# Performance work log

Hardware: AMD Instinct MI355X
Metric: run time of the kernel (lower is better)

The kernel has to match this reference:

```python
import jax, jax.numpy as jnp
import numpy as np
import math

B, T, C = 4, 2048, 1024
H = 16
D = C // H

def setup_inputs() -> dict:
    key = jax.random.key(0)
    k1, k2, k3 = jax.random.split(key, 3)
    x = jax.random.normal(k1, (B, T, C), dtype=jnp.float32)
    w_attn = jax.random.normal(k2, (3 * C, C), dtype=jnp.float32) * (1.0 / math.sqrt(C))
    b_attn = jnp.zeros((3 * C,), dtype=jnp.float32)
    w_proj = jax.random.normal(k3, (C, C), dtype=jnp.float32) * (1.0 / math.sqrt(C))
    b_proj = jnp.zeros((C,), dtype=jnp.float32)
    return {"x": x, "w_attn": w_attn, "b_attn": b_attn, "w_proj": w_proj, "b_proj": b_proj}

def reference(x, w_attn, b_attn, w_proj, b_proj):
    Bq, Tq, Cq = x.shape
    qkv = x @ w_attn.T + b_attn                      # [B,T,3C]
    q, k, v = jnp.split(qkv, 3, axis=-1)
    q = q.reshape(Bq, Tq, H, D).transpose(0, 2, 1, 3)  # [B,H,T,D]
    k = k.reshape(Bq, Tq, H, D).transpose(0, 2, 1, 3)
    v = v.reshape(Bq, Tq, H, D).transpose(0, 2, 1, 3)
    att = jnp.einsum('bhqd,bhkd->bhqk', q, k) * (1.0 / math.sqrt(D))
    causal = jnp.tril(jnp.ones((Tq, Tq), dtype=bool))
    att = jnp.where(causal[None, None], att, -jnp.inf)
    att = jax.nn.softmax(att, axis=-1)
    y = jnp.einsum('bhqk,bhkd->bhqd', att, v)          # [B,H,T,D]
    y = y.transpose(0, 2, 1, 3).reshape(Bq, Tq, Cq)
    return y @ w_proj.T + b_proj
```

## Files before the change

kernel.cpp:

```cpp
#include <hip/hip_runtime.h>
#include <hip/hip_bf16.h>


typedef __hip_bfloat16 bf16;
typedef __attribute__((ext_vector_type(8))) short bf16x8;
typedef __attribute__((ext_vector_type(4))) float f32x4;
typedef __attribute__((ext_vector_type(16))) float f32x16;

#define MFMA16(a, b, c) __builtin_amdgcn_mfma_f32_16x16x32_bf16(a, b, c, 0, 0, 0)
#define MFMA32(a, b, c) __builtin_amdgcn_mfma_f32_32x32x16_bf16(a, b, c, 0, 0, 0)
#define GLOAD_LDS(g, l) __builtin_amdgcn_global_load_lds( \
    (const __attribute__((address_space(1))) void*)(g),    \
    (__attribute__((address_space(3))) void*)(l), 16, 0, 0)

constexpr int Bn = 4, Tn = 2048, Cn = 1024, Hn = 16, Dn = 64;
constexpr size_t HT_ELEMS = (size_t)64 * Tn * Dn;
constexpr float QSCALE = 0.18033688011112042f;

__device__ __forceinline__ short f2bf(float f) {
    unsigned u = __float_as_uint(f);
    return (short)((u + 0x7FFF + ((u >> 16) & 1)) >> 16);
}
__device__ __forceinline__ bf16 bfbits(short s) { bf16 b; __builtin_memcpy(&b, &s, 2); return b; }

__device__ __forceinline__ unsigned cvtpk_bf16(float lo, float hi) {
    unsigned r;
    asm("v_cvt_pk_bf16_f32 %0, %1, %2" : "=v"(r) : "v"(lo), "v"(hi));
    return r;
}
__device__ __forceinline__ void permswap(unsigned& a, unsigned& b) {
#if __has_builtin(__builtin_amdgcn_permlane32_swap)
    auto r = __builtin_amdgcn_permlane32_swap(a, b, false, false);
    a = (unsigned)r[0]; b = (unsigned)r[1];
#else
    asm("v_permlane32_swap_b32 %0, %1" : "+v"(a), "+v"(b));
#endif
}
__device__ __forceinline__ bf16x8 pack4(unsigned w0, unsigned w1, unsigned w2, unsigned w3) {
    union { unsigned u[4]; bf16x8 v; } t;
    t.u[0] = w0; t.u[1] = w1; t.u[2] = w2; t.u[3] = w3;
    return t.v;
}

__global__ __launch_bounds__(256) void cast3_kernel(
    const float* __restrict__ x, const float* __restrict__ wa,
    const float* __restrict__ wp, bf16* __restrict__ out)
{
    size_t i = (size_t)blockIdx.x * 256 + threadIdx.x;
    const float* src; size_t off;
    if (i < 1048576)      { src = x;  off = i; }
    else if (i < 1441792) { src = wa; off = i - 1048576; }
    else                  { src = wp; off = i - 1441792; }
    const float4* p = (const float4*)(src + off * 8);
    float4 a = p[0], b = p[1];
    bf16x8 r;
    r[0] = f2bf(a.x); r[1] = f2bf(a.y); r[2] = f2bf(a.z); r[3] = f2bf(a.w);
    r[4] = f2bf(b.x); r[5] = f2bf(b.y); r[6] = f2bf(b.z); r[7] = f2bf(b.w);
    *(bf16x8*)(out + i * 8) = r;
}

__global__ __launch_bounds__(256) void qkv_gemm128(
    const bf16* __restrict__ Am, const bf16* __restrict__ Wm,
    const float* __restrict__ bias,
    bf16* __restrict__ qo, bf16* __restrict__ ko, bf16* __restrict__ vo)
{
    constexpr int K = 1024;
    __shared__ bf16 As[4096], Bs[4096];
    const int tid = threadIdx.x;
    const int lane = tid & 63, w = tid >> 6;
    const int row = lane & 15, quad = lane >> 4;
    const unsigned bid = blockIdx.x;
    const int x8 = bid & 7, l = bid >> 3;
    const int tm = (x8 >> 1) * 16 + l / 12;
    const int tn = (x8 & 1) * 12 + l % 12;
    const int m0 = tm * 128, n0 = tn * 128;

    const int srow = tid >> 2, skch = tid & 3;
    const bf16* ag0 = Am + (size_t)(m0 + srow) * K + skch * 8;
    const bf16* ag1 = ag0 + (size_t)64 * K;
    const bf16* wg0 = Wm + (size_t)(n0 + srow) * K + skch * 8;
    const bf16* wg1 = wg0 + (size_t)64 * K;
    bf16* asl0 = As + tid * 8;  bf16* asl1 = As + 2048 + tid * 8;
    bf16* bsl0 = Bs + tid * 8;  bf16* bsl1 = Bs + 2048 + tid * 8;

    f32x4 acc[4][4];
    #pragma unroll
    for (int i = 0; i < 4; i++)
        #pragma unroll
        for (int j = 0; j < 4; j++) acc[i][j] = {0, 0, 0, 0};

    const int r0 = (w >> 1) * 64, c0 = (w & 1) * 64;

    for (int k0 = 0; k0 < K; k0 += 32) {
        __syncthreads();
        GLOAD_LDS(ag0 + k0, asl0);
        GLOAD_LDS(ag1 + k0, asl1);
        GLOAD_LDS(wg0 + k0, bsl0);
        GLOAD_LDS(wg1 + k0, bsl1);
        __syncthreads();
        bf16x8 af[4], bfv[4];
        #pragma unroll
        for (int it = 0; it < 4; it++)
            af[it] = *(const bf16x8*)(As + (r0 + it * 16 + row) * 32 + quad * 8);
        #pragma unroll
        for (int jt = 0; jt < 4; jt++)
            bfv[jt] = *(const bf16x8*)(Bs + (c0 + jt * 16 + row) * 32 + quad * 8);
        #pragma unroll
        for (int it = 0; it < 4; it++)
            #pragma unroll
            for (int jt = 0; jt < 4; jt++)
                acc[it][jt] = MFMA16(af[it], bfv[jt], acc[it][jt]);
    }

    #pragma unroll
    for (int it = 0; it < 4; it++)
    #pragma unroll
    for (int jt = 0; jt < 4; jt++)
    #pragma unroll
    for (int r = 0; r < 4; r++) {
        int m = m0 + r0 + it * 16 + quad * 4 + r;
        int n = n0 + c0 + jt * 16 + row;
        float val = acc[it][jt][r] + bias[n];
        int which = n >> 10, cc = n & 1023;
        if (which == 0) val *= QSCALE;
        bf16 bv = bfbits(f2bf(val));
        int h = cc >> 6, d = cc & 63;
        int b = m >> 11, t = m & 2047;
        int bh = b * Hn + h;
        if (which == 0)      qo[((size_t)bh * Tn + t) * Dn + d] = bv;
        else if (which == 1) ko[((size_t)bh * Tn + t) * Dn + d] = bv;
        else                 vo[((size_t)bh * 64 + (t >> 5)) * 2048 + (size_t)d * 32 + (t & 31)] = bv;
    }
}

__global__ __launch_bounds__(256, 4) void attn_kernel(
    const bf16* __restrict__ qbp, const bf16* __restrict__ kbp,
    const bf16* __restrict__ vtb, bf16* __restrict__ ob)
{
    __shared__ __align__(128) bf16 SB[4][2048];
    __shared__ float lbufw[4][32];
    const int tid  = threadIdx.x;
    const int lane = tid & 63;
    const int w    = tid >> 6;
    const int l31  = lane & 31, hl = lane >> 5;
    const int bid  = blockIdx.x;
    const int qid  = bid & 7;
    const int idx  = bid >> 3;
    const int bh   = qid * 8 + (idx & 7);
    const int pair = idx >> 3;

    const int stage_off = w * 1024 + (lane >> 3) * 128
                        + (((lane & 7) ^ ((lane >> 3) & 7)) << 4);
    const int kxor = (l31 & 7) << 4;
    const int sxor = ((l31 >> 1) & 7) << 4;

    const bf16* Q  = qbp + (size_t)bh * Tn * Dn;
    const char* Kh = (const char*)(kbp + (size_t)bh * Tn * Dn);
    const char* Vh = (const char*)vtb + (size_t)bh * 262144;

    #pragma unroll 1
    for (int sub = 0; sub < 2; sub++) {
        const int qb8  = sub ? (15 - pair) : pair;
        const int jmax = qb8 * 4 + 3;
        const int qtw  = qb8 * 4 + w;
        const int q0w  = qtw * 32;

        bf16x8 bQ[4];
        {
            const bf16* qp = Q + (size_t)(q0w + l31) * Dn + hl * 8;
            #pragma unroll
            for (int kf = 0; kf < 4; kf++) bQ[kf] = *(const bf16x8*)(qp + kf * 16);
        }

        f32x16 o2[2];
        o2[0] = {0,0,0,0,0,0,0,0,0,0,0,0,0,0,0,0};
        o2[1] = {0,0,0,0,0,0,0,0,0,0,0,0,0,0,0,0};
        float lsum = 0.f;

        GLOAD_LDS(Kh + stage_off, (char*)SB[0] + w * 1024);
        GLOAD_LDS(Vh + stage_off, (char*)SB[2] + w * 1024);
        __syncthreads();

        for (int j = 0; j <= jmax; j++) {
            const int cur = j & 1;
            if (j < jmax) {
                const int nb = cur ^ 1;
                GLOAD_LDS(Kh + (size_t)(j + 1) * 4096 + stage_off, (char*)SB[nb] + w * 1024);
                GLOAD_LDS(Vh + (size_t)(j + 1) * 4096 + stage_off, (char*)SB[2 + nb] + w * 1024);
            }
            if (j <= qtw) {
                const char* KB = (const char*)SB[cur];
                const char* VB = (const char*)SB[2 + cur];
                bf16x8 aK[4];
                #pragma unroll
                for (int kf = 0; kf < 4; kf++)
                    aK[kf] = *(const bf16x8*)(KB + l31 * 128 + ((((kf * 2 + hl)) << 4) ^ kxor));

                f32x16 s = {0,0,0,0,0,0,0,0,0,0,0,0,0,0,0,0};
                __builtin_amdgcn_s_setprio(1);
                s = MFMA32(aK[0], bQ[0], s);
                s = MFMA32(aK[1], bQ[1], s);
                s = MFMA32(aK[2], bQ[2], s);
                s = MFMA32(aK[3], bQ[3], s);
                __builtin_amdgcn_s_setprio(0);

                bf16x8 vf[4];
                #pragma unroll
                for (int i2 = 0; i2 < 4; i2++) {
                    const int vh = i2 >> 1, kc = i2 & 1;
                    const int stripe = vh * 16 + (l31 >> 1);
                    vf[i2] = *(const bf16x8*)(VB + stripe * 128
                              + ((((l31 & 1) * 4 + kc * 2 + hl) << 4) ^ sxor));
                }

                float p[16];
                if (j == qtw) {
                    #pragma unroll
                    for (int r = 0; r < 16; r++) {
                        const int krow = (r & 3) + 8 * (r >> 2) + 4 * hl;
                        float e = exp2f(s[r]);
                        p[r] = (krow > l31) ? 0.f : e;
                    }
                } else {
                    #pragma unroll
                    for (int r = 0; r < 16; r++) p[r] = exp2f(s[r]);
                }
                lsum += (((p[0]+p[1]) + (p[2]+p[3])) + ((p[4]+p[5]) + (p[6]+p[7])))
                      + (((p[8]+p[9]) + (p[10]+p[11])) + ((p[12]+p[13]) + (p[14]+p[15])));

                unsigned a0 = cvtpk_bf16(p[0],  p[1]),  b0 = cvtpk_bf16(p[4],  p[5]);
                unsigned a1 = cvtpk_bf16(p[2],  p[3]),  b1 = cvtpk_bf16(p[6],  p[7]);
                unsigned a2 = cvtpk_bf16(p[8],  p[9]),  b2 = cvtpk_bf16(p[12], p[13]);
                unsigned a3 = cvtpk_bf16(p[10], p[11]), b3 = cvtpk_bf16(p[14], p[15]);
                permswap(a0, b0);
                permswap(a1, b1);
                permswap(a2, b2);
                permswap(a3, b3);
                const bf16x8 P0 = pack4(a0, a1, b0, b1);
                const bf16x8 P1 = pack4(a2, a3, b2, b3);

                __builtin_amdgcn_s_setprio(1);
                o2[0] = MFMA32(P0, vf[0], o2[0]);
                o2[0] = MFMA32(P1, vf[1], o2[0]);
                o2[1] = MFMA32(P0, vf[2], o2[1]);
                o2[1] = MFMA32(P1, vf[3], o2[1]);
                __builtin_amdgcn_s_setprio(0);
            }
            __syncthreads();
        }

        unsigned lsu = __float_as_uint(lsum), lsv = lsu;
        permswap(lsu, lsv);
        const float ltot = __uint_as_float(lsu) + __uint_as_float(lsv);
        if (hl == 0) lbufw[w][l31] = 1.0f / ltot;
        asm volatile("s_waitcnt lgkmcnt(0)" ::: "memory");

        char* obl = (char*)SB[w];
        #pragma unroll
        for (int r = 0; r < 16; r++) {
            const int q  = (r & 3) + 8 * (r >> 2) + 4 * hl;
            const float rl = lbufw[w][q];
            const int qx = (q & 7) << 4;
            *(short*)(obl + q * 128 + ((2 * l31) ^ qx))      = f2bf(o2[0][r] * rl);
            *(short*)(obl + q * 128 + ((64 + 2 * l31) ^ qx)) = f2bf(o2[1][r] * rl);
        }
        asm volatile("s_waitcnt lgkmcnt(0)" ::: "memory");

        {
            const int q = lane >> 1, half = lane & 1;
            const int qx = (q & 7) << 4;
            const int b = bh >> 4, h = bh & 15;
            bf16* gdst = ob + ((size_t)(b * Tn + (q0w + q))) * Cn + h * Dn + half * 32;
            #pragma unroll
            for (int c = 0; c < 4; c++) {
                bf16x8 rv = *(const bf16x8*)(obl + q * 128 + (((half * 64) + c * 16) ^ qx));
                *(bf16x8*)(gdst + c * 8) = rv;
            }
        }
        __syncthreads();
    }
}

__global__ __launch_bounds__(256) void proj_gemm128(
    const bf16* __restrict__ Am, const bf16* __restrict__ Wm,
    const float* __restrict__ bias, float* __restrict__ out)
{
    constexpr int K = 1024;
    __shared__ bf16 As[4096], Bs[4096];
    const int tid = threadIdx.x;
    const int lane = tid & 63, w = tid >> 6;
    const int row = lane & 15, quad = lane >> 4;
    const unsigned bid = blockIdx.x;
    const int x8 = bid & 7, l = bid >> 3;
    const int tm = x8 * 8 + l / 8;
    const int tn = l % 8;
    const int m0 = tm * 128, n0 = tn * 128;

    const int srow = tid >> 2, skch = tid & 3;
    const bf16* ag0 = Am + (size_t)(m0 + srow) * K + skch * 8;
    const bf16* ag1 = ag0 + (size_t)64 * K;
    const bf16* wg0 = Wm + (size_t)(n0 + srow) * K + skch * 8;
    const bf16* wg1 = wg0 + (size_t)64 * K;
    bf16* asl0 = As + tid * 8;  bf16* asl1 = As + 2048 + tid * 8;
    bf16* bsl0 = Bs + tid * 8;  bf16* bsl1 = Bs + 2048 + tid * 8;

    f32x4 acc[4][4];
    #pragma unroll
    for (int i = 0; i < 4; i++)
        #pragma unroll
        for (int j = 0; j < 4; j++) acc[i][j] = {0, 0, 0, 0};

    const int r0 = (w >> 1) * 64, c0 = (w & 1) * 64;

    for (int k0 = 0; k0 < K; k0 += 32) {
        __syncthreads();
        GLOAD_LDS(ag0 + k0, asl0);
        GLOAD_LDS(ag1 + k0, asl1);
        GLOAD_LDS(wg0 + k0, bsl0);
        GLOAD_LDS(wg1 + k0, bsl1);
        __syncthreads();
        bf16x8 af[4], bfv[4];
        #pragma unroll
        for (int it = 0; it < 4; it++)
            af[it] = *(const bf16x8*)(As + (r0 + it * 16 + row) * 32 + quad * 8);
        #pragma unroll
        for (int jt = 0; jt < 4; jt++)
            bfv[jt] = *(const bf16x8*)(Bs + (c0 + jt * 16 + row) * 32 + quad * 8);
        #pragma unroll
        for (int it = 0; it < 4; it++)
            #pragma unroll
            for (int jt = 0; jt < 4; jt++)
                acc[it][jt] = MFMA16(af[it], bfv[jt], acc[it][jt]);
    }

    #pragma unroll
    for (int it = 0; it < 4; it++)
    #pragma unroll
    for (int jt = 0; jt < 4; jt++)
    #pragma unroll
    for (int r = 0; r < 4; r++) {
        int m = m0 + r0 + it * 16 + quad * 4 + r;
        int n = n0 + c0 + jt * 16 + row;
        out[(size_t)m * 1024 + n] = acc[it][jt][r] + bias[n];
    }
}

extern "C" void kernel_launch(void* const* d_in, const int* in_sizes, int n_in,
                              void* d_out, int out_size, void* d_ws, size_t ws_size,
                              hipStream_t stream) {
    const float* x      = (const float*)d_in[0];
    const float* w_attn = (const float*)d_in[1];
    const float* b_attn = (const float*)d_in[2];
    const float* w_proj = (const float*)d_in[3];
    const float* b_proj = (const float*)d_in[4];
    float* out = (float*)d_out;

    bf16* ws  = (bf16*)((char*)d_ws + 1024);
    bf16* xb  = ws;
    bf16* wab = xb  + (size_t)8192 * 1024;
    bf16* wpb = wab + (size_t)3072 * 1024;
    bf16* q   = wpb + (size_t)1024 * 1024;
    bf16* k   = q  + HT_ELEMS;
    bf16* vt  = k  + HT_ELEMS;
    bf16* o   = vt + HT_ELEMS;

    cast3_kernel<<<6144, 256, 0, stream>>>(x, w_attn, w_proj, xb);

    qkv_gemm128 <<<64 * 24, 256, 0, stream>>>(xb, wab, b_attn, q, k, vt);
    attn_kernel <<<512, 256, 0, stream>>>(q, k, vt, o);
    proj_gemm128<<<64 * 8, 256, 0, stream>>>(o, wpb, b_proj, out);
}
```

Before: 296.7 us.

## Process two 32-key tiles per attention loop iteration to halve barriers

The attention kernel now stages 64 keys of K and V per iteration instead of 32. LDS buffers double and each wave issues four global-to-LDS loads. Each iteration runs two QK/PV sub-blocks, with causal masking and skipping handled per sub-tile. This halves the __syncthreads and loop overhead per key and gives more MFMA work between barriers. In exchange it doubles LDS use, increases register pressure, and relaxes launch bounds from 4 to 2 blocks per SIMD, which may lower occupancy.

Result: faster. 289.1 us (-2.6%).

```diff
diff --git a/kernel.cpp b/kernel.cpp
--- a/kernel.cpp
+++ b/kernel.cpp
@@ -133,11 +133,11 @@
     }
 }
 
-__global__ __launch_bounds__(256, 4) void attn_kernel(
+__global__ __launch_bounds__(256, 2) void attn_kernel(
     const bf16* __restrict__ qbp, const bf16* __restrict__ kbp,
     const bf16* __restrict__ vtb, bf16* __restrict__ ob)
 {
-    __shared__ __align__(128) bf16 SB[4][2048];
+    __shared__ __align__(128) bf16 SB[4][4096];
     __shared__ float lbufw[4][32];
     const int tid  = threadIdx.x;
     const int lane = tid & 63;
@@ -149,8 +149,8 @@
     const int bh   = qid * 8 + (idx & 7);
     const int pair = idx >> 3;
 
-    const int stage_off = w * 1024 + (lane >> 3) * 128
-                        + (((lane & 7) ^ ((lane >> 3) & 7)) << 4);
+    const int s2off = w * 2048 + (lane >> 3) * 128
+                    + (((lane & 7) ^ ((lane >> 3) & 7)) << 4);
     const int kxor = (l31 & 7) << 4;
     const int sxor = ((l31 >> 1) & 7) << 4;
 
@@ -160,10 +160,12 @@
 
     #pragma unroll 1
     for (int sub = 0; sub < 2; sub++) {
-        const int qb8  = sub ? (15 - pair) : pair;
-        const int jmax = qb8 * 4 + 3;
-        const int qtw  = qb8 * 4 + w;
-        const int q0w  = qtw * 32;
+        const int qb8   = sub ? (15 - pair) : pair;
+        const int jmax2 = qb8 * 2 + 1;
+        const int qtw   = qb8 * 4 + w;
+        const int q0w   = qtw * 32;
+        const int jd    = qtw >> 1;
+        const int par   = qtw & 1;
 
         bf16x8 bQ[4];
         {
@@ -177,74 +179,117 @@
         o2[1] = {0,0,0,0,0,0,0,0,0,0,0,0,0,0,0,0};
         float lsum = 0.f;
 
-        GLOAD_LDS(Kh + stage_off, (char*)SB[0] + w * 1024);
-        GLOAD_LDS(Vh + stage_off, (char*)SB[2] + w * 1024);
-        __syncthreads();
-
-        for (int j = 0; j <= jmax; j++) {
+        GLOAD_LDS(Kh + s2off,        (char*)SB[0] + w * 2048);
+        GLOAD_LDS(Kh + s2off + 1024, (char*)SB[0] + w * 2048 + 1024);
+        GLOAD_LDS(Vh + s2off,        (char*)SB[2] + w * 2048);
+        GLOAD_LDS(Vh + s2off + 1024, (char*)SB[2] + w * 2048 + 1024);
+        __syncthreads();
+
+        for (int j = 0; j <= jmax2; j++) {
             const int cur = j & 1;
-            if (j < jmax) {
+            if (j < jmax2) {
                 const int nb = cur ^ 1;
-                GLOAD_LDS(Kh + (size_t)(j + 1) * 4096 + stage_off, (char*)SB[nb] + w * 1024);
-                GLOAD_LDS(Vh + (size_t)(j + 1) * 4096 + stage_off, (char*)SB[2 + nb] + w * 1024);
+                const size_t go = (size_t)(j + 1) * 8192;
+                GLOAD_LDS(Kh + go + s2off,        (char*)SB[nb] + w * 2048);
+                GLOAD_LDS(Kh + go + s2off + 1024, (char*)SB[nb] + w * 2048 + 1024);
+                GLOAD_LDS(Vh + go + s2off,        (char*)SB[2 + nb] + w * 2048);
+                GLOAD_LDS(Vh + go + s2off + 1024, (char*)SB[2 + nb] + w * 2048 + 1024);
             }
-            if (j <= qtw) {
+            if (j <= jd) {
                 const char* KB = (const char*)SB[cur];
                 const char* VB = (const char*)SB[2 + cur];
-                bf16x8 aK[4];
+                const bool doB = (j < jd) || par;
+
+                bf16x8 aKa[4], aKb[4];
                 #pragma unroll
-                for (int kf = 0; kf < 4; kf++)
-                    aK[kf] = *(const bf16x8*)(KB + l31 * 128 + ((((kf * 2 + hl)) << 4) ^ kxor));
-
-                f32x16 s = {0,0,0,0,0,0,0,0,0,0,0,0,0,0,0,0};
+                for (int kf = 0; kf < 4; kf++) {
+                    const int co = ((kf * 2 + hl) << 4) ^ kxor;
+                    aKa[kf] = *(const bf16x8*)(KB + l31 * 128 + co);
+                    aKb[kf] = *(const bf16x8*)(KB + 4096 + l31 * 128 + co);
+                }
+
+                f32x16 sA = {0,0,0,0,0,0,0,0,0,0,0,0,0,0,0,0};
+                f32x16 sB = {0,0,0,0,0,0,0,0,0,0,0,0,0,0,0,0};
                 __builtin_amdgcn_s_setprio(1);
-                s = MFMA32(aK[0], bQ[0], s);
-                s = MFMA32(aK[1], bQ[1], s);
-                s = MFMA32(aK[2], bQ[2], s);
-                s = MFMA32(aK[3], bQ[3], s);
+                #pragma unroll
+                for (int kf = 0; kf < 4; kf++) sA = MFMA32(aKa[kf], bQ[kf], sA);
+                if (doB) {
+                    #pragma unroll
+                    for (int kf = 0; kf < 4; kf++) sB = MFMA32(aKb[kf], bQ[kf], sB);
+                }
                 __builtin_amdgcn_s_setprio(0);
 
-                bf16x8 vf[4];
+                bf16x8 vfL[4], vfH[4];
                 #pragma unroll
                 for (int i2 = 0; i2 < 4; i2++) {
                     const int vh = i2 >> 1, kc = i2 & 1;
-                    const int stripe = vh * 16 + (l31 >> 1);
-                    vf[i2] = *(const bf16x8*)(VB + stripe * 128
-                              + ((((l31 & 1) * 4 + kc * 2 + hl) << 4) ^ sxor));
+                    const int off = (vh * 16 + (l31 >> 1)) * 128
+                                  + ((((l31 & 1) * 4 + kc * 2 + hl) << 4) ^ sxor);
+                    vfL[i2] = *(const bf16x8*)(VB + off);
+                    if (doB) vfH[i2] = *(const bf16x8*)(VB + 4096 + off);
                 }
 
-                float p[16];
-                if (j == qtw) {
+                float pA[16];
+                if (j == jd && par == 0) {
                     #pragma unroll
                     for (int r = 0; r < 16; r++) {
                         const int krow = (r & 3) + 8 * (r >> 2) + 4 * hl;
-                        float e = exp2f(s[r]);
-                        p[r] = (krow > l31) ? 0.f : e;
+                        float e = exp2f(sA[r]);
+                        pA[r] = (krow > l31) ? 0.f : e;
                     }
                 } else {
                     #pragma unroll
-                    for (int r = 0; r < 16; r++) p[r] = exp2f(s[r]);
+                    for (int r = 0; r < 16; r++) pA[r] = exp2f(sA[r]);
                 }
-                lsum += (((p[0]+p[1]) + (p[2]+p[3])) + ((p[4]+p[5]) + (p[6]+p[7])))
-                      + (((p[8]+p[9]) + (p[10]+p[11])) + ((p[12]+p[13]) + (p[14]+p[15])));
-
-                unsigned a0 = cvtpk_bf16(p[0],  p[1]),  b0 = cvtpk_bf16(p[4],  p[5]);
-                unsigned a1 = cvtpk_bf16(p[2],  p[3]),  b1 = cvtpk_bf16(p[6],  p[7]);
-                unsigned a2 = cvtpk_bf16(p[8],  p[9]),  b2 = cvtpk_bf16(p[12], p[13]);
-                unsigned a3 = cvtpk_bf16(p[10], p[11]), b3 = cvtpk_bf16(p[14], p[15]);
-                permswap(a0, b0);
-                permswap(a1, b1);
-                permswap(a2, b2);
-                permswap(a3, b3);
-                const bf16x8 P0 = pack4(a0, a1, b0, b1);
-                const bf16x8 P1 = pack4(a2, a3, b2, b3);
+                lsum += (((pA[0]+pA[1]) + (pA[2]+pA[3])) + ((pA[4]+pA[5]) + (pA[6]+pA[7])))
+                      + (((pA[8]+pA[9]) + (pA[10]+pA[11])) + ((pA[12]+pA[13]) + (pA[14]+pA[15])));
+
+                unsigned a0 = cvtpk_bf16(pA[0],  pA[1]),  b0 = cvtpk_bf16(pA[4],  pA[5]);
+                unsigned a1 = cvtpk_bf16(pA[2],  pA[3]),  b1 = cvtpk_bf16(pA[6],  pA[7]);
+                unsigned a2 = cvtpk_bf16(pA[8],  pA[9]),  b2 = cvtpk_bf16(pA[12], pA[13]);
+                unsigned a3 = cvtpk_bf16(pA[10], pA[11]), b3 = cvtpk_bf16(pA[14], pA[15]);
+                permswap(a0, b0); permswap(a1, b1); permswap(a2, b2); permswap(a3, b3);
+                const bf16x8 PA0 = pack4(a0, a1, b0, b1);
+                const bf16x8 PA1 = pack4(a2, a3, b2, b3);
 
                 __builtin_amdgcn_s_setprio(1);
-                o2[0] = MFMA32(P0, vf[0], o2[0]);
-                o2[0] = MFMA32(P1, vf[1], o2[0]);
-                o2[1] = MFMA32(P0, vf[2], o2[1]);
-                o2[1] = MFMA32(P1, vf[3], o2[1]);
+                o2[0] = MFMA32(PA0, vfL[0], o2[0]);
+                o2[0] = MFMA32(PA1, vfL[1], o2[0]);
+                o2[1] = MFMA32(PA0, vfL[2], o2[1]);
+                o2[1] = MFMA32(PA1, vfL[3], o2[1]);
                 __builtin_amdgcn_s_setprio(0);
+
+                if (doB) {
+                    float pB[16];
+                    if (j == jd) {
+                        #pragma unroll
+                        for (int r = 0; r < 16; r++) {
+                            const int krow = (r & 3) + 8 * (r >> 2) + 4 * hl;
+                            float e = exp2f(sB[r]);
+                            pB[r] = (krow > l31) ? 0.f : e;
+                        }
+                    } else {
+                        #pragma unroll
+                        for (int r = 0; r < 16; r++) pB[r] = exp2f(sB[r]);
+                    }
+                    lsum += (((pB[0]+pB[1]) + (pB[2]+pB[3])) + ((pB[4]+pB[5]) + (pB[6]+pB[7])))
+                          + (((pB[8]+pB[9]) + (pB[10]+pB[11])) + ((pB[12]+pB[13]) + (pB[14]+pB[15])));
+
+                    unsigned c0_ = cvtpk_bf16(pB[0],  pB[1]),  d0_ = cvtpk_bf16(pB[4],  pB[5]);
+                    unsigned c1_ = cvtpk_bf16(pB[2],  pB[3]),  d1_ = cvtpk_bf16(pB[6],  pB[7]);
+                    unsigned c2_ = cvtpk_bf16(pB[8],  pB[9]),  d2_ = cvtpk_bf16(pB[12], pB[13]);
+                    unsigned c3_ = cvtpk_bf16(pB[10], pB[11]), d3_ = cvtpk_bf16(pB[14], pB[15]);
+                    permswap(c0_, d0_); permswap(c1_, d1_); permswap(c2_, d2_); permswap(c3_, d3_);
+                    const bf16x8 PB0 = pack4(c0_, c1_, d0_, d1_);
+                    const bf16x8 PB1 = pack4(c2_, c3_, d2_, d3_);
+
+                    __builtin_amdgcn_s_setprio(1);
+                    o2[0] = MFMA32(PB0, vfH[0], o2[0]);
+                    o2[0] = MFMA32(PB1, vfH[1], o2[0]);
+                    o2[1] = MFMA32(PB0, vfH[2], o2[1]);
+                    o2[1] = MFMA32(PB1, vfH[3], o2[1]);
+                    __builtin_amdgcn_s_setprio(0);
+                }
             }
             __syncthreads();
         }
```
